# Kernel optimization log

Hardware: AMD Instinct MI355X
Metric: run time of the kernel (lower is better)

The kernel has to match this reference:

```python
import jax, jax.numpy as jnp
import numpy as np

D_MODEL = 1024
N_HEADS = 16
HEAD_DIM = D_MODEL // N_HEADS


def _rotary_tables(seq_len, dim):
    # sin/cos tables: (seq_len, dim//2)
    pos = jnp.arange(seq_len, dtype=jnp.float32)[:, None]
    freqs = 1.0 / 10000.0 ** (jnp.arange(0, dim, 2, dtype=jnp.float32) / dim)
    angles = pos * freqs
    return jnp.sin(angles), jnp.cos(angles)


def _apply_rotary(x, sin, cos):
    # x: (B, H, N, head_dim); sin/cos: (N, head_dim//2) broadcast over B,H
    d_half = x.shape[-1] // 2
    x1, x2 = x[..., :d_half], x[..., d_half:]
    return jnp.concatenate([x1 * cos - x2 * sin, x1 * sin + x2 * cos], axis=-1)


def setup_inputs() -> dict:
    key = jax.random.key(0)
    k_x, k_q, k_k, k_v, k_o = jax.random.split(key, 5)
    B, N = 4, 2048
    scale = 1.0 / np.sqrt(D_MODEL)
    return {
        "x": jax.random.normal(k_x, (B, N, D_MODEL), dtype=jnp.float32),
        "Wq": jax.random.normal(k_q, (D_MODEL, D_MODEL), dtype=jnp.float32) * scale,
        "Wk": jax.random.normal(k_k, (D_MODEL, D_MODEL), dtype=jnp.float32) * scale,
        "Wv": jax.random.normal(k_v, (D_MODEL, D_MODEL), dtype=jnp.float32) * scale,
        "Wo": jax.random.normal(k_o, (D_MODEL, D_MODEL), dtype=jnp.float32) * scale,
    }


def reference(x, Wq, Wk, Wv, Wo):
    B, N, _ = x.shape
    # nn.Linear(d, d, bias=False): y = x @ W.T ; view+transpose -> (B, H, N, hd)
    def proj(W):
        return jnp.einsum('bnd,ed->bne', x, W).reshape(B, N, N_HEADS, HEAD_DIM).transpose(0, 2, 1, 3)

    Q, K, V = proj(Wq), proj(Wk), proj(Wv)
    sin, cos = _rotary_tables(N, HEAD_DIM)
    Q = _apply_rotary(Q, sin, cos)
    K = _apply_rotary(K, sin, cos)

    # SDPA (non-causal, dropout=0): softmax(Q K^T / sqrt(hd)) V
    scores = jnp.einsum('bhqd,bhkd->bhqk', Q, K) / jnp.sqrt(jnp.asarray(HEAD_DIM, x.dtype))
    attn = jax.nn.softmax(scores, axis=-1)
    out = jnp.einsum('bhqk,bhkd->bhqd', attn, V)  # (B, H, N, hd)
    out = out.transpose(0, 2, 1, 3).reshape(B, N, D_MODEL)
    return jnp.einsum('bnd,ed->bne', out, Wo)
```

## Files before the change

### kernel.cpp

```cpp
#include <hip/hip_runtime.h>
#include <stdint.h>

#define SEQ    2048
#define DMODEL 1024
#define NHEADS 16
#define HDIM   64
#define BATCH  4
#define MTOT   (BATCH*SEQ)

typedef __attribute__((ext_vector_type(8)))  short s16x8;
typedef __attribute__((ext_vector_type(4)))  short s16x4;
typedef __attribute__((ext_vector_type(4)))  float f32x4;
typedef __attribute__((ext_vector_type(16))) float f32x16;

#define OFF_SIN  ((size_t)0)
#define OFF_COS  ((size_t)262144)
#define OFF_XHI  ((size_t)524288)
#define OFF_WQH  ((size_t)34078720)
#define OFF_WKH  ((size_t)38273024)
#define OFF_WVH  ((size_t)42467328)
#define OFF_WOH  ((size_t)46661632)
#define OFF_QR   ((size_t)50855936)
#define OFF_KR   ((size_t)67633152)
#define OFF_VT   ((size_t)84410368)
#define OFF_AHI  ((size_t)101187584)

#define QSCALE 0.18033688011112042f

__device__ __forceinline__ uint16_t f2bf(float f){
  union{float f;uint32_t u;}v; v.f=f;
  uint32_t r=v.u+0x7fffu+((v.u>>16)&1u);
  return (uint16_t)(r>>16);
}
__device__ __forceinline__ float bf2f(uint16_t u){
  union{uint32_t u;float f;}v; v.u=((uint32_t)u)<<16; return v.f;
}

__device__ __forceinline__ void async16(void* lds, const void* g){
  __builtin_amdgcn_global_load_lds(
    (const __attribute__((address_space(1))) void*)g,
    (__attribute__((address_space(3))) void*)lds, 16, 0, 0);
}

__device__ __forceinline__ float fexp2(float x){
#if __has_builtin(__builtin_amdgcn_exp2f)
  return __builtin_amdgcn_exp2f(x);
#else
  float r; asm("v_exp_f32 %0, %1" : "=v"(r) : "v"(x)); return r;
#endif
}
__device__ __forceinline__ float frcp(float x){
#if __has_builtin(__builtin_amdgcn_rcpf)
  return __builtin_amdgcn_rcpf(x);
#else
  float r; asm("v_rcp_f32 %0, %1" : "=v"(r) : "v"(x)); return r;
#endif
}
__device__ __forceinline__ void plswap(unsigned a, unsigned b, unsigned &o0, unsigned &o1){
#if __has_builtin(__builtin_amdgcn_permlane32_swap)
  auto r = __builtin_amdgcn_permlane32_swap(a, b, false, false);
  o0 = (unsigned)r[0]; o1 = (unsigned)r[1];
#else
  unsigned ax = (unsigned)__shfl_xor((int)a, 32, 64);
  unsigned bx = (unsigned)__shfl_xor((int)b, 32, 64);
  bool hi = (threadIdx.x & 32) != 0;
  o0 = hi ? bx : a;
  o1 = hi ? b  : ax;
#endif
}

__global__ __launch_bounds__(256) void prep_k(
  const float* __restrict__ x,
  const float* __restrict__ Wq, const float* __restrict__ Wk,
  const float* __restrict__ Wv, const float* __restrict__ Wo,
  uint16_t* __restrict__ xhi, uint16_t* __restrict__ wqh, uint16_t* __restrict__ wkh,
  uint16_t* __restrict__ wvh, uint16_t* __restrict__ woh,
  float* __restrict__ st, float* __restrict__ ct)
{
  int b = blockIdx.x;
  if (b < 12288){
    const float* s; uint16_t* d; int i;
    if (b < 8192){ s = x; d = xhi; i = b*256 + threadIdx.x; }
    else {
      int wsel = (b - 8192) >> 10;
      int lb   = (b - 8192) & 1023;
      s = wsel==0? Wq : wsel==1? Wk : wsel==2? Wv : Wo;
      d = wsel==0? wqh: wsel==1? wkh: wsel==2? wvh: woh;
      i = lb*256 + threadIdx.x;
    }
    f32x4 v = *(const f32x4*)(s + (size_t)i*4);
    s16x4 vh;
    #pragma unroll
    for(int r=0;r<4;r++) vh[r] = (short)f2bf(v[r]);
    *(s16x4*)(d + (size_t)i*4) = vh;
  } else {
    int i = (b - 12288)*256 + threadIdx.x;
    int n = i>>5, j = i&31;
    double freq = pow(10000.0, -(double)j/32.0);
    double ang = (double)n*freq;
    st[i] = (float)sin(ang);
    ct[i] = (float)cos(ang);
  }
}

__device__ __forceinline__ void gemm_mainloop64(
  const uint16_t* __restrict__ A, const uint16_t* __restrict__ B,
  int m0, int e0, char* lA, char* lB, f32x4 acc[4][4])
{
  const int t = threadIdx.x;
  const int lane = t & 63;
  const int wr = t>>7, wc = (t>>6)&1;
  const int lq = lane&15, lg = lane>>4;
  const int rowA = wr*64 + lq;
  const int rowB = wc*64 + lq;

  int dbyte[4], srow[4], sbyte[4];
  #pragma unroll
  for (int s=0;s<4;s++){
    int d = s*4096 + t*16;
    int r = d>>7, c = (d>>4)&7;
    dbyte[s]=d; srow[s]=r; sbyte[s]=(c ^ (r&7))*16;
  }
  int chh[2];
  #pragma unroll
  for (int kh=0;kh<2;kh++) chh[kh] = (((kh<<2)|lg) ^ (lq&7))*16;

  const char* Ab = (const char*)A;
  const char* Bb = (const char*)B;

  for (int k0=0; k0<DMODEL; k0+=64){
    #pragma unroll
    for (int s=0;s<4;s++){
      async16(lA + dbyte[s], Ab + (size_t)(m0+srow[s])*2048 + k0*2 + sbyte[s]);
      async16(lB + dbyte[s], Bb + (size_t)(e0+srow[s])*2048 + k0*2 + sbyte[s]);
    }
    __syncthreads();
    #pragma unroll
    for (int kh=0;kh<2;kh++){
      s16x8 af[4], bfr[4];
      #pragma unroll
      for (int mi=0;mi<4;mi++) af[mi]  = *(const s16x8*)(lA + (rowA+mi*16)*128 + chh[kh]);
      #pragma unroll
      for (int ni=0;ni<4;ni++) bfr[ni] = *(const s16x8*)(lB + (rowB+ni*16)*128 + chh[kh]);
      __builtin_amdgcn_s_setprio(1);
      #pragma unroll
      for (int mi=0;mi<4;mi++){
        #pragma unroll
        for (int ni=0;ni<4;ni++)
          acc[mi][ni] = __builtin_amdgcn_mfma_f32_16x16x32_bf16(af[mi], bfr[ni], acc[mi][ni],0,0,0);
      }
      __builtin_amdgcn_s_setprio(0);
    }
    __syncthreads();
  }
}

__global__ __launch_bounds__(256) void gemm_qkv_k(
  const uint16_t* __restrict__ Xh,
  const uint16_t* __restrict__ WqH, const uint16_t* __restrict__ WkH, const uint16_t* __restrict__ WvH,
  const float* __restrict__ st, const float* __restrict__ ct,
  uint16_t* __restrict__ Qr, uint16_t* __restrict__ Kr, uint16_t* __restrict__ Vt)
{
  __shared__ char lA[128*128], lB[128*128];
  int m0 = blockIdx.x*128;
  int cti = blockIdx.y;
  int seg = cti>>3;
  int e0 = (cti&7)*128;
  const uint16_t* W = seg==0? WqH : (seg==1? WkH : WvH);
  f32x4 acc[4][4];
  #pragma unroll
  for(int i=0;i<4;i++){
    #pragma unroll
    for(int j=0;j<4;j++) acc[i][j] = (f32x4){0.f,0.f,0.f,0.f};
  }
  gemm_mainloop64(Xh, W, m0, e0, lA, lB, acc);

  int t=threadIdx.x, lane=t&63, lq=lane&15, lg=lane>>4;
  int wr=t>>7, wc=(t>>6)&1;
  int eb = e0 + wc*64;
  int h = eb>>6;
  int rbase = m0 + wr*64 + lg*4;
  if (seg<2){
    uint16_t* O = seg==0? Qr:Kr;
    float qs = seg==0 ? QSCALE : 1.0f;
    #pragma unroll
    for(int mi=0;mi<4;mi++){
      #pragma unroll
      for(int ni=0;ni<2;ni++){
        int j = ni*16+lq;
        #pragma unroll
        for(int r=0;r<4;r++){
          int m = rbase + mi*16 + r;
          int b = m>>11, n = m&2047;
          float sv = st[n*32+j], cv = ct[n*32+j];
          float x1 = acc[mi][ni][r], x2 = acc[mi][ni+2][r];
          size_t base = ((size_t)((b*NHEADS+h)*SEQ + n))*HDIM;
          O[base + j]      = f2bf((x1*cv - x2*sv)*qs);
          O[base + j + 32] = f2bf((x1*sv + x2*cv)*qs);
        }
      }
    }
  } else {
    #pragma unroll
    for(int mi=0;mi<4;mi++){
      #pragma unroll
      for(int ni=0;ni<4;ni++){
        int dh = ni*16+lq;
        int m = rbase + mi*16;
        int b = m>>11, n = m&2047;
        s16x4 v;
        #pragma unroll
        for(int r=0;r<4;r++) v[r] = (short)f2bf(acc[mi][ni][r]);
        *(s16x4*)(Vt + ((size_t)((b*NHEADS+h)*HDIM + dh))*SEQ + n) = v;
      }
    }
  }
}

__global__ __launch_bounds__(256) void attn_k(
  const uint16_t* __restrict__ Qr, const uint16_t* __restrict__ Kr, const uint16_t* __restrict__ Vt,
  uint16_t* __restrict__ Ah)
{
  __shared__ uint16_t ldsK[3][64*64];
  __shared__ uint16_t ldsV[3][64*64];

  int bid = blockIdx.x;
  int w = (bid & 7)*128 + (bid >> 3);
  int bh = w >> 4, qt = w & 15;
  int tid = threadIdx.x;
  int wid = tid >> 6, lane = tid & 63;
  int l31 = lane & 31, hi = lane >> 5;
  int q0 = qt*128 + wid*32;

  const uint16_t* Qb = Qr + (size_t)bh*SEQ*HDIM;
  const uint16_t* Kb = Kr + (size_t)bh*SEQ*HDIM;
  const uint16_t* Vb = Vt + (size_t)bh*HDIM*SEQ;

  s16x8 qf[4];
  #pragma unroll
  for (int sp=0; sp<4; ++sp)
    qf[sp] = *(const s16x8*)(Qb + (size_t)(q0 + l31)*HDIM + sp*16 + hi*8);

  s16x8 ones;
  #pragma unroll
  for (int j=0;j<8;j++) ones[j] = (short)0x3F80;

  f32x16 zm16;
  #pragma unroll
  for (int r=0;r<16;r++) zm16[r] = -16.0f;

  f32x16 oa[2], lacc;
  #pragma unroll
  for (int r=0;r<16;r++){ oa[0][r]=0.f; oa[1][r]=0.f; lacc[r]=0.f; }

  const int e7 = l31 & 7;
  const int rK = l31*128;
  const int kOff[4]  = { (((0+hi)^e7)<<4), (((2+hi)^e7)<<4), (((4+hi)^e7)<<4), (((6+hi)^e7)<<4) };
  const int vOff0[2] = { (((0+hi)^e7)<<4), (((2+hi)^e7)<<4) };
  const int vOff1[2] = { (((4+hi)^e7)<<4), (((6+hi)^e7)<<4) };

  auto STAGE = [&](int buf, int t){
    const char* Ks = (const char*)(Kb + (size_t)t*64*HDIM);
    char* dK = (char*)&ldsK[buf][0];
    char* dV = (char*)&ldsV[buf][0];
    #pragma unroll
    for (int r=0; r<2; ++r){
      int ci = r*256 + tid;
      int sc = ci ^ ((ci>>3)&7);
      async16(dK + ci*16, Ks + sc*16);
    }
    #pragma unroll
    for (int r=0; r<2; ++r){
      int ci = r*256 + tid;
      int row = ci>>3;
      int sc = (ci&7) ^ (row&7);
      async16(dV + ci*16, (const char*)Vb + ((size_t)row*SEQ + (size_t)t*64)*2 + sc*16);
    }
  };

  STAGE(0, 0);
  STAGE(1, 1);
  asm volatile("s_waitcnt vmcnt(4)" ::: "memory");
  __syncthreads();

  const int NT = SEQ/64;
  int cur = 0;
  for (int t=0; t<NT; ++t){
    int nxt2 = cur+2; if (nxt2>=3) nxt2-=3;
    if (t+2 < NT) STAGE(nxt2, t+2);
    const char* bK = (const char*)&ldsK[cur][0];
    const char* bV = (const char*)&ldsV[cur][0];

    s16x8 kf0[4], kf1[4];
    #pragma unroll
    for (int sp=0; sp<4; ++sp){
      kf0[sp] = *(const s16x8*)(bK + rK + kOff[sp]);
      kf1[sp] = *(const s16x8*)(bK + 4096 + rK + kOff[sp]);
    }
    f32x16 sacc0 = zm16, sacc1 = zm16;
    __builtin_amdgcn_s_setprio(1);
    #pragma unroll
    for (int sp=0; sp<4; ++sp)
      sacc0 = __builtin_amdgcn_mfma_f32_32x32x16_bf16(kf0[sp], qf[sp], sacc0, 0,0,0);
    #pragma unroll
    for (int sp=0; sp<4; ++sp)
      sacc1 = __builtin_amdgcn_mfma_f32_32x32x16_bf16(kf1[sp], qf[sp], sacc1, 0,0,0);
    __builtin_amdgcn_s_setprio(0);

    s16x8 vf0[4];
    #pragma unroll
    for (int db=0; db<2; ++db)
      #pragma unroll
      for (int s=0; s<2; ++s)
        vf0[db*2+s] = *(const s16x8*)(bV + db*4096 + rK + vOff0[s]);

    float p[16];
    #pragma unroll
    for (int r=0;r<16;r++) p[r] = fexp2(sacc0[r]);
    uint32_t pw[8];
    #pragma unroll
    for (int j=0;j<8;j++)
      asm("v_cvt_pk_bf16_f32 %0, %1, %2" : "=v"(pw[j]) : "v"(p[2*j]), "v"(p[2*j+1]));
    unsigned w0,w1,w2,w3, x0,x1,x2,x3;
    plswap(pw[0], pw[2], w0, w2);
    plswap(pw[1], pw[3], w1, w3);
    plswap(pw[4], pw[6], x0, x2);
    plswap(pw[5], pw[7], x1, x3);
    union { uint32_t wd[4]; s16x8 v; } pa0, pa1;
    pa0.wd[0]=w0; pa0.wd[1]=w1; pa0.wd[2]=w2; pa0.wd[3]=w3;
    pa1.wd[0]=x0; pa1.wd[1]=x1; pa1.wd[2]=x2; pa1.wd[3]=x3;
    __builtin_amdgcn_s_setprio(1);
    #pragma unroll
    for (int db=0; db<2; ++db){
      oa[db] = __builtin_amdgcn_mfma_f32_32x32x16_bf16(pa0.v, vf0[db*2+0], oa[db], 0,0,0);
      oa[db] = __builtin_amdgcn_mfma_f32_32x32x16_bf16(pa1.v, vf0[db*2+1], oa[db], 0,0,0);
    }
    lacc = __builtin_amdgcn_mfma_f32_32x32x16_bf16(pa0.v, ones, lacc, 0,0,0);
    lacc = __builtin_amdgcn_mfma_f32_32x32x16_bf16(pa1.v, ones, lacc, 0,0,0);
    __builtin_amdgcn_s_setprio(0);

    s16x8 vf1[4];
    #pragma unroll
    for (int db=0; db<2; ++db)
      #pragma unroll
      for (int s=0; s<2; ++s)
        vf1[db*2+s] = *(const s16x8*)(bV + db*4096 + rK + vOff1[s]);

    #pragma unroll
    for (int r=0;r<16;r++) p[r] = fexp2(sacc1[r]);
    #pragma unroll
    for (int j=0;j<8;j++)
      asm("v_cvt_pk_bf16_f32 %0, %1, %2" : "=v"(pw[j]) : "v"(p[2*j]), "v"(p[2*j+1]));
    plswap(pw[0], pw[2], w0, w2);
    plswap(pw[1], pw[3], w1, w3);
    plswap(pw[4], pw[6], x0, x2);
    plswap(pw[5], pw[7], x1, x3);
    pa0.wd[0]=w0; pa0.wd[1]=w1; pa0.wd[2]=w2; pa0.wd[3]=w3;
    pa1.wd[0]=x0; pa1.wd[1]=x1; pa1.wd[2]=x2; pa1.wd[3]=x3;
    __builtin_amdgcn_s_setprio(1);
    #pragma unroll
    for (int db=0; db<2; ++db){
      oa[db] = __builtin_amdgcn_mfma_f32_32x32x16_bf16(pa0.v, vf1[db*2+0], oa[db], 0,0,0);
      oa[db] = __builtin_amdgcn_mfma_f32_32x32x16_bf16(pa1.v, vf1[db*2+1], oa[db], 0,0,0);
    }
    lacc = __builtin_amdgcn_mfma_f32_32x32x16_bf16(pa0.v, ones, lacc, 0,0,0);
    lacc = __builtin_amdgcn_mfma_f32_32x32x16_bf16(pa1.v, ones, lacc, 0,0,0);
    __builtin_amdgcn_s_setprio(0);

    if (t+2 < NT)      asm volatile("s_waitcnt vmcnt(4)" ::: "memory");
    else if (t+1 < NT) asm volatile("s_waitcnt vmcnt(0)" ::: "memory");
    if (t+1 < NT)      asm volatile("s_barrier" ::: "memory");
    cur = cur+1; if (cur>=3) cur-=3;
  }

  int b = bh >> 4, h = bh & 15;
  #pragma unroll
  for (int r=0;r<16;r++){
    int q = (r&3) + 8*(r>>2) + 4*hi;
    float inv = frcp(lacc[r]);
    size_t mrow = ((size_t)(b*SEQ + q0 + q))*DMODEL + (size_t)h*HDIM + l31;
    #pragma unroll
    for (int db=0; db<2; ++db)
      Ah[mrow + db*32] = f2bf(oa[db][r]*inv);
  }
}

__global__ __launch_bounds__(256) void gemm_out_k(
  const uint16_t* __restrict__ Ahp, const uint16_t* __restrict__ WoH, float* __restrict__ C)
{
  __shared__ char lA[128*128], lB[128*128];
  int m0 = blockIdx.x*128;
  int e0 = blockIdx.y*128;
  f32x4 acc[4][4];
  #pragma unroll
  for(int i=0;i<4;i++){
    #pragma unroll
    for(int j=0;j<4;j++) acc[i][j] = (f32x4){0.f,0.f,0.f,0.f};
  }
  gemm_mainloop64(Ahp, WoH, m0, e0, lA, lB, acc);
  int t=threadIdx.x, lane=t&63, lq=lane&15, lg=lane>>4;
  int wr=t>>7, wc=(t>>6)&1;
  int rbase = m0 + wr*64 + lg*4;
  int cb = e0 + wc*64;
  #pragma unroll
  for(int mi=0;mi<4;mi++){
    #pragma unroll
    for(int ni=0;ni<4;ni++){
      #pragma unroll
      for(int r=0;r<4;r++)
        C[(size_t)(rbase+mi*16+r)*DMODEL + cb + ni*16 + lq] = acc[mi][ni][r];
    }
  }
}

extern "C" void kernel_launch(void* const* d_in, const int* in_sizes, int n_in,
                              void* d_out, int out_size, void* d_ws, size_t ws_size,
                              hipStream_t stream) {
  const float* x  = (const float*)d_in[0];
  const float* Wq = (const float*)d_in[1];
  const float* Wk = (const float*)d_in[2];
  const float* Wv = (const float*)d_in[3];
  const float* Wo = (const float*)d_in[4];
  float* out = (float*)d_out;
  char* ws = (char*)d_ws;

  float* sin_t = (float*)(ws + OFF_SIN);
  float* cos_t = (float*)(ws + OFF_COS);
  uint16_t* xhi = (uint16_t*)(ws + OFF_XHI);
  uint16_t* wqh = (uint16_t*)(ws + OFF_WQH);
  uint16_t* wkh = (uint16_t*)(ws + OFF_WKH);
  uint16_t* wvh = (uint16_t*)(ws + OFF_WVH);
  uint16_t* woh = (uint16_t*)(ws + OFF_WOH);
  uint16_t* Qr  = (uint16_t*)(ws + OFF_QR);
  uint16_t* Kr  = (uint16_t*)(ws + OFF_KR);
  uint16_t* Vt  = (uint16_t*)(ws + OFF_VT);
  uint16_t* ahi = (uint16_t*)(ws + OFF_AHI);

  prep_k<<<dim3(12544),dim3(256),0,stream>>>(x, Wq, Wk, Wv, Wo,
                                             xhi, wqh, wkh, wvh, woh, sin_t, cos_t);

  gemm_qkv_k<<<dim3(MTOT/128, 24),dim3(256),0,stream>>>(xhi, wqh, wkh, wvh,
                                                        sin_t, cos_t, Qr, Kr, Vt);
  attn_k<<<dim3(BATCH*NHEADS*(SEQ/128)),dim3(256),0,stream>>>(Qr, Kr, Vt, ahi);
  gemm_out_k<<<dim3(MTOT/128, 8),dim3(256),0,stream>>>(ahi, woh, out);
}
```

Baseline: 201.2 us.

## Switch attention K/V staging to double buffer and stagger half-tile order across waves

Cuts the attention kernel's LDS staging from triple to double buffering (48KB to 32KB of shared memory) and waits for all loads at the end of each tile instead of keeping two tiles in flight. Odd waves process the second 32-key half of each tile first, so waves read different LDS regions at the same time and avoid bank contention. The main cost removed is LDS footprint, which may allow more blocks per CU, plus bank conflicts. The risk is a shallower prefetch pipeline, so global load latency is less well hidden.

```diff
diff --git a/kernel.cpp b/kernel.cpp
--- a/kernel.cpp
+++ b/kernel.cpp
@@ -221,8 +221,7 @@
   const uint16_t* __restrict__ Qr, const uint16_t* __restrict__ Kr, const uint16_t* __restrict__ Vt,
   uint16_t* __restrict__ Ah)
 {
-  __shared__ uint16_t ldsK[3][64*64];
-  __shared__ uint16_t ldsV[3][64*64];
+  __shared__ char lds[32768];
 
   int bid = blockIdx.x;
   int w = (bid & 7)*128 + (bid >> 3);
@@ -256,13 +255,17 @@
   const int e7 = l31 & 7;
   const int rK = l31*128;
   const int kOff[4]  = { (((0+hi)^e7)<<4), (((2+hi)^e7)<<4), (((4+hi)^e7)<<4), (((6+hi)^e7)<<4) };
-  const int vOff0[2] = { (((0+hi)^e7)<<4), (((2+hi)^e7)<<4) };
-  const int vOff1[2] = { (((4+hi)^e7)<<4), (((6+hi)^e7)<<4) };
+  const int vA0 = (((0+hi)^e7)<<4), vA1 = (((2+hi)^e7)<<4);
+  const int vB0 = (((4+hi)^e7)<<4), vB1 = (((6+hi)^e7)<<4);
+  const bool odd = (wid & 1) != 0;
+  const int kBaseF = odd ? 4096 : 0,   kBaseS = odd ? 0 : 4096;
+  const int vF0 = odd ? vB0 : vA0,     vF1 = odd ? vB1 : vA1;
+  const int vS0 = odd ? vA0 : vB0,     vS1 = odd ? vA1 : vB1;
 
   auto STAGE = [&](int buf, int t){
     const char* Ks = (const char*)(Kb + (size_t)t*64*HDIM);
-    char* dK = (char*)&ldsK[buf][0];
-    char* dV = (char*)&ldsV[buf][0];
+    char* dK = lds + buf*8192;
+    char* dV = lds + 16384 + buf*8192;
     #pragma unroll
     for (int r=0; r<2; ++r){
       int ci = r*256 + tid;
@@ -278,45 +281,26 @@
     }
   };
 
-  STAGE(0, 0);
-  STAGE(1, 1);
-  asm volatile("s_waitcnt vmcnt(4)" ::: "memory");
-  __syncthreads();
-
-  const int NT = SEQ/64;
-  int cur = 0;
-  for (int t=0; t<NT; ++t){
-    int nxt2 = cur+2; if (nxt2>=3) nxt2-=3;
-    if (t+2 < NT) STAGE(nxt2, t+2);
-    const char* bK = (const char*)&ldsK[cur][0];
-    const char* bV = (const char*)&ldsV[cur][0];
-
-    s16x8 kf0[4], kf1[4];
-    #pragma unroll
-    for (int sp=0; sp<4; ++sp){
-      kf0[sp] = *(const s16x8*)(bK + rK + kOff[sp]);
-      kf1[sp] = *(const s16x8*)(bK + 4096 + rK + kOff[sp]);
-    }
-    f32x16 sacc0 = zm16, sacc1 = zm16;
+  auto SUBSTEP = [&](const char* bK, const char* bV, int kbase, int v0, int v1){
+    s16x8 kf[4];
+    #pragma unroll
+    for (int sp=0; sp<4; ++sp)
+      kf[sp] = *(const s16x8*)(bK + kbase + rK + kOff[sp]);
+    f32x16 sacc = zm16;
     __builtin_amdgcn_s_setprio(1);
     #pragma unroll
     for (int sp=0; sp<4; ++sp)
-      sacc0 = __builtin_amdgcn_mfma_f32_32x32x16_bf16(kf0[sp], qf[sp], sacc0, 0,0,0);
-    #pragma unroll
-    for (int sp=0; sp<4; ++sp)
-      sacc1 = __builtin_amdgcn_mfma_f32_32x32x16_bf16(kf1[sp], qf[sp], sacc1, 0,0,0);
+      sacc = __builtin_amdgcn_mfma_f32_32x32x16_bf16(kf[sp], qf[sp], sacc, 0,0,0);
     __builtin_amdgcn_s_setprio(0);
-
-    s16x8 vf0[4];
-    #pragma unroll
-    for (int db=0; db<2; ++db)
-      #pragma unroll
-      for (int s=0; s<2; ++s)
-        vf0[db*2+s] = *(const s16x8*)(bV + db*4096 + rK + vOff0[s]);
-
+    s16x8 vf[4];
+    #pragma unroll
+    for (int db=0; db<2; ++db){
+      vf[db*2+0] = *(const s16x8*)(bV + db*4096 + rK + v0);
+      vf[db*2+1] = *(const s16x8*)(bV + db*4096 + rK + v1);
+    }
     float p[16];
     #pragma unroll
-    for (int r=0;r<16;r++) p[r] = fexp2(sacc0[r]);
+    for (int r=0;r<16;r++) p[r] = fexp2(sacc[r]);
     uint32_t pw[8];
     #pragma unroll
     for (int j=0;j<8;j++)
@@ -330,47 +314,29 @@
     pa0.wd[0]=w0; pa0.wd[1]=w1; pa0.wd[2]=w2; pa0.wd[3]=w3;
     pa1.wd[0]=x0; pa1.wd[1]=x1; pa1.wd[2]=x2; pa1.wd[3]=x3;
     __builtin_amdgcn_s_setprio(1);
-    #pragma unroll
-    for (int db=0; db<2; ++db){
-      oa[db] = __builtin_amdgcn_mfma_f32_32x32x16_bf16(pa0.v, vf0[db*2+0], oa[db], 0,0,0);
-      oa[db] = __builtin_amdgcn_mfma_f32_32x32x16_bf16(pa1.v, vf0[db*2+1], oa[db], 0,0,0);
-    }
+    oa[0] = __builtin_amdgcn_mfma_f32_32x32x16_bf16(pa0.v, vf[0], oa[0], 0,0,0);
+    oa[0] = __builtin_amdgcn_mfma_f32_32x32x16_bf16(pa1.v, vf[1], oa[0], 0,0,0);
+    oa[1] = __builtin_amdgcn_mfma_f32_32x32x16_bf16(pa0.v, vf[2], oa[1], 0,0,0);
+    oa[1] = __builtin_amdgcn_mfma_f32_32x32x16_bf16(pa1.v, vf[3], oa[1], 0,0,0);
     lacc = __builtin_amdgcn_mfma_f32_32x32x16_bf16(pa0.v, ones, lacc, 0,0,0);
     lacc = __builtin_amdgcn_mfma_f32_32x32x16_bf16(pa1.v, ones, lacc, 0,0,0);
     __builtin_amdgcn_s_setprio(0);
-
-    s16x8 vf1[4];
-    #pragma unroll
-    for (int db=0; db<2; ++db)
-      #pragma unroll
-      for (int s=0; s<2; ++s)
-        vf1[db*2+s] = *(const s16x8*)(bV + db*4096 + rK + vOff1[s]);
-
-    #pragma unroll
-    for (int r=0;r<16;r++) p[r] = fexp2(sacc1[r]);
-    #pragma unroll
-    for (int j=0;j<8;j++)
-      asm("v_cvt_pk_bf16_f32 %0, %1, %2" : "=v"(pw[j]) : "v"(p[2*j]), "v"(p[2*j+1]));
-    plswap(pw[0], pw[2], w0, w2);
-    plswap(pw[1], pw[3], w1, w3);
-    plswap(pw[4], pw[6], x0, x2);
-    plswap(pw[5], pw[7], x1, x3);
-    pa0.wd[0]=w0; pa0.wd[1]=w1; pa0.wd[2]=w2; pa0.wd[3]=w3;
-    pa1.wd[0]=x0; pa1.wd[1]=x1; pa1.wd[2]=x2; pa1.wd[3]=x3;
-    __builtin_amdgcn_s_setprio(1);
-    #pragma unroll
-    for (int db=0; db<2; ++db){
-      oa[db] = __builtin_amdgcn_mfma_f32_32x32x16_bf16(pa0.v, vf1[db*2+0], oa[db], 0,0,0);
-      oa[db] = __builtin_amdgcn_mfma_f32_32x32x16_bf16(pa1.v, vf1[db*2+1], oa[db], 0,0,0);
-    }
-    lacc = __builtin_amdgcn_mfma_f32_32x32x16_bf16(pa0.v, ones, lacc, 0,0,0);
-    lacc = __builtin_amdgcn_mfma_f32_32x32x16_bf16(pa1.v, ones, lacc, 0,0,0);
-    __builtin_amdgcn_s_setprio(0);
-
-    if (t+2 < NT)      asm volatile("s_waitcnt vmcnt(4)" ::: "memory");
-    else if (t+1 < NT) asm volatile("s_waitcnt vmcnt(0)" ::: "memory");
-    if (t+1 < NT)      asm volatile("s_barrier" ::: "memory");
-    cur = cur+1; if (cur>=3) cur-=3;
+  };
+
+  STAGE(0, 0);
+  asm volatile("s_waitcnt vmcnt(0)" ::: "memory");
+  __syncthreads();
+
+  const int NT = SEQ/64;
+  for (int t=0; t<NT; ++t){
+    int cur = t & 1;
+    if (t+1 < NT) STAGE(cur^1, t+1);
+    const char* bK = lds + cur*8192;
+    const char* bV = lds + 16384 + cur*8192;
+    SUBSTEP(bK, bV, kBaseF, vF0, vF1);
+    SUBSTEP(bK, bV, kBaseS, vS0, vS1);
+    asm volatile("s_waitcnt vmcnt(0)" ::: "memory");
+    __syncthreads();
   }
 
   int b = bh >> 4, h = bh & 15;
```

After: 198.4 us. Within noise of the previous version (-1.4%).
